# Optimization experiments

Measured on AMD Instinct MI355X. Metric: run time of the kernel, lower is better.

## Reference

```python
import jax, jax.numpy as jnp
import numpy as np

EMBED_DIM = 1024
NUM_HEADS = 16
HEAD_DIM = EMBED_DIM // NUM_HEADS


def setup_inputs() -> dict:
    key = jax.random.key(0)
    ks = jax.random.split(key, 11)
    B, S, E = 4, 2048, EMBED_DIM
    s = 1.0 / np.sqrt(E)
    return {
        "query": jax.random.normal(ks[0], (B, S, E), jnp.float32),
        "key": jax.random.normal(ks[1], (B, S, E), jnp.float32),
        "value": jax.random.normal(ks[2], (B, S, E), jnp.float32),
        "Wq": jax.random.normal(ks[3], (E, E), jnp.float32) * s,
        "bq": jnp.zeros((E,), jnp.float32),
        "Wk": jax.random.normal(ks[4], (E, E), jnp.float32) * s,
        "bk": jnp.zeros((E,), jnp.float32),
        "Wv": jax.random.normal(ks[5], (E, E), jnp.float32) * s,
        "bv": jnp.zeros((E,), jnp.float32),
        "Wo": jax.random.normal(ks[6], (E, E), jnp.float32) * s,
        "bo": jnp.zeros((E,), jnp.float32),
    }


def reference(query, key, value, Wq, bq, Wk, bk, Wv, bv, Wo, bo):
    B, S, E = query.shape
    H, D = NUM_HEADS, HEAD_DIM
    scale = jnp.float32(np.sqrt(D))
    # linear projections (torch Linear: x @ W.T + b)
    Q = (query @ Wq.T + bq).reshape(B, S, H, D).transpose(0, 2, 1, 3)  # [B,H,S,D]
    K = (key @ Wk.T + bk).reshape(B, S, H, D).transpose(0, 2, 1, 3)
    V = (value @ Wv.T + bv).reshape(B, S, H, D).transpose(0, 2, 1, 3)
    # full O(S^2) score materialization, matching the eager torch code
    scores = jnp.einsum("bhqd,bhkd->bhqk", Q, K) / scale  # [B,H,S,S]
    attn = jax.nn.softmax(scores, axis=-1)
    out = jnp.einsum("bhqk,bhkd->bhqd", attn, V)  # [B,H,S,D]
    out = out.transpose(0, 2, 1, 3).reshape(B, S, E)
    out = out @ Wo.T + bo
    return out, attn.mean(axis=1)
```

## Files before the change

### kernel.cpp

```cpp
#include <hip/hip_runtime.h>
#include <hip/hip_bf16.h>

#define DEVI __device__ __forceinline__

typedef __bf16 bf16x8 __attribute__((ext_vector_type(8)));
typedef __bf16 bf16x4 __attribute__((ext_vector_type(4)));
typedef float f32x4 __attribute__((ext_vector_type(4)));

constexpr int B_ = 4, S_ = 2048, E_ = 1024, H_ = 16, D_ = 64;
constexpr int N_ = B_ * S_;
constexpr float SC2_ = 0.18033688011112042f;

constexpr size_t XB_OFF = 0;
constexpr size_t WB_OFF = 50331648;
constexpr size_t QB_OFF = 58720256;
constexpr size_t KB_OFF = 75497472;
constexpr size_t VT_OFF = 92274688;
constexpr size_t CTX_OFF = 109051904;
constexpr size_t LS_OFF = 125829120;
constexpr size_t WS_NEED = 126353408;

typedef const __attribute__((address_space(1))) void* gas_ptr;
typedef __attribute__((address_space(3))) void* las_ptr;

DEVI void load_lds16(const void* g, void* l) {
  __builtin_amdgcn_global_load_lds((gas_ptr)g, (las_ptr)l, 16, 0, 0);
}

DEVI f32x4 mfma16(bf16x8 a, bf16x8 b, f32x4 c) {
  return __builtin_amdgcn_mfma_f32_16x16x32_bf16(a, b, c, 0, 0, 0);
}

DEVI int swz(int row) { return ((row >> 1) ^ (row >> 3)) & 3; }

#if __has_builtin(__builtin_amdgcn_exp2f)
DEVI float ex2(float x) { return __builtin_amdgcn_exp2f(x); }
#else
DEVI float ex2(float x) { return exp2f(x); }
#endif

__global__ __launch_bounds__(256) void conv_x(const float* __restrict__ q,
                                              const float* __restrict__ k,
                                              const float* __restrict__ v,
                                              __bf16* __restrict__ dst) {
  const float* src = (blockIdx.y == 0) ? q : ((blockIdx.y == 1) ? k : v);
  __bf16* d = dst + (size_t)blockIdx.y * N_ * E_;
  size_t i = ((size_t)blockIdx.x * blockDim.x + threadIdx.x) * 4;
  float4 f = *(const float4*)(src + i);
  bf16x4 o;
  o[0] = (__bf16)f.x; o[1] = (__bf16)f.y; o[2] = (__bf16)f.z; o[3] = (__bf16)f.w;
  *(bf16x4*)(d + i) = o;
}

__global__ __launch_bounds__(256) void conv_w(const float* __restrict__ wq,
                                              const float* __restrict__ wk,
                                              const float* __restrict__ wv,
                                              const float* __restrict__ wo,
                                              __bf16* __restrict__ dst) {
  const float* src = (blockIdx.y == 0) ? wq : ((blockIdx.y == 1) ? wk :
                     ((blockIdx.y == 2) ? wv : wo));
  __bf16* d = dst + (size_t)blockIdx.y * E_ * E_;
  size_t i = ((size_t)blockIdx.x * blockDim.x + threadIdx.x) * 4;
  float4 f = *(const float4*)(src + i);
  bf16x4 o;
  o[0] = (__bf16)f.x; o[1] = (__bf16)f.y; o[2] = (__bf16)f.z; o[3] = (__bf16)f.w;
  *(bf16x4*)(d + i) = o;
}

__global__ __launch_bounds__(256) void gemm_qkv(const __bf16* __restrict__ Xb,
                                                const __bf16* __restrict__ Wb,
                                                const float* __restrict__ bq,
                                                const float* __restrict__ bk,
                                                const float* __restrict__ bv,
                                                __bf16* __restrict__ Qb,
                                                __bf16* __restrict__ Kb,
                                                __bf16* __restrict__ Vt) {
  __shared__ __attribute__((aligned(16))) __bf16 As[128 * 32];
  __shared__ __attribute__((aligned(16))) __bf16 Bs[128 * 32];
  const int z = blockIdx.z;
  const __bf16* A = Xb + (size_t)z * N_ * E_;
  const __bf16* W = Wb + (size_t)z * E_ * E_;
  const float* bias = (z == 0) ? bq : ((z == 1) ? bk : bv);
  const int m0 = blockIdx.x * 128, n0 = blockIdx.y * 128;
  const int t = threadIdx.x, lane = t & 63, w = t >> 6;
  const int wm = w >> 1, wn = w & 1;
  const int l15 = lane & 15, g = lane >> 4;

  f32x4 acc[4][4] = {};

  for (int kk = 0; kk < E_; kk += 32) {
#pragma unroll
    for (int i = 0; i < 2; ++i) {
      int c = t + i * 256;
      int row = c >> 2, kc = c & 3;
      int sl = kc ^ swz(row);
      load_lds16(A + (size_t)(m0 + row) * E_ + kk + sl * 8, (void*)(As + c * 8));
      load_lds16(W + (size_t)(n0 + row) * E_ + kk + sl * 8, (void*)(Bs + c * 8));
    }
    __syncthreads();
    bf16x8 a[4], b[4];
#pragma unroll
    for (int i = 0; i < 4; ++i) {
      int row = wm * 64 + i * 16 + l15;
      a[i] = *(const bf16x8*)(As + row * 32 + (g ^ swz(row)) * 8);
    }
#pragma unroll
    for (int j = 0; j < 4; ++j) {
      int row = wn * 64 + j * 16 + l15;
      b[j] = *(const bf16x8*)(Bs + row * 32 + (g ^ swz(row)) * 8);
    }
#pragma unroll
    for (int i = 0; i < 4; ++i)
#pragma unroll
      for (int j = 0; j < 4; ++j)
        acc[i][j] = mfma16(a[i], b[j], acc[i][j]);
    __syncthreads();
  }

#pragma unroll
  for (int i = 0; i < 4; ++i) {
    int mloc = wm * 64 + i * 16 + (g << 2);
#pragma unroll
    for (int j = 0; j < 4; ++j) {
      int nloc = wn * 64 + j * 16 + l15;
      int n = n0 + nloc;
      int h = n >> 6, d = n & 63;
      float bs = bias[n];
      if (z == 2) {
        int m = m0 + mloc;
        int bb = m >> 11, s = m & 2047;
        bf16x4 pk;
#pragma unroll
        for (int r = 0; r < 4; ++r) pk[r] = (__bf16)(acc[i][j][r] + bs);
        *(bf16x4*)(Vt + ((size_t)(bb * H_ + h) * D_ + d) * S_ + s) = pk;
      } else {
        __bf16* dst = (z == 0) ? Qb : Kb;
#pragma unroll
        for (int r = 0; r < 4; ++r) {
          int m = m0 + mloc + r;
          int bb = m >> 11, s = m & 2047;
          dst[((size_t)(bb * H_ + h) * S_ + s) * D_ + d] = (__bf16)(acc[i][j][r] + bs);
        }
      }
    }
  }
}

__global__ __launch_bounds__(256, 4) void attn_pv(const __bf16* __restrict__ Qb,
                                                  const __bf16* __restrict__ Kb,
                                                  const __bf16* __restrict__ Vt,
                                                  float* __restrict__ Lsum,
                                                  __bf16* __restrict__ Ctx) {
  __shared__ __attribute__((aligned(16))) __bf16 Qs[2 * 128 * 32];
  __shared__ __attribute__((aligned(16))) __bf16 Ks[2 * 64 * 32];
  __shared__ __attribute__((aligned(16))) __bf16 Vs[2 * 64 * 32];

  const int q0 = blockIdx.x * 128;
  const int bh = blockIdx.y;
  const __bf16* Qh = Qb + (size_t)bh * S_ * D_;
  const __bf16* Kh = Kb + (size_t)bh * S_ * D_;
  const __bf16* Vh = Vt + (size_t)bh * D_ * S_;
  const int t = threadIdx.x, lane = t & 63, w = t >> 6;
  const int l15 = lane & 15, g = lane >> 4;
  const int ksel = 8 * (l15 >> 2) + (l15 & 3);

#pragma unroll
  for (int i = 0; i < 4; ++i) {
    int c = t + i * 256;
    int sub = c >> 9, rem = c & 511, row = rem >> 2, kc = rem & 3;
    int sl = kc ^ swz(row);
    load_lds16(Qh + (size_t)(q0 + row) * D_ + sub * 32 + sl * 8, (void*)(Qs + c * 8));
  }
  __syncthreads();
  bf16x8 qf[2][2];
#pragma unroll
  for (int jb = 0; jb < 2; ++jb) {
    int row = w * 32 + jb * 16 + l15;
#pragma unroll
    for (int ks = 0; ks < 2; ++ks)
      qf[jb][ks] = *(const bf16x8*)(Qs + ks * 4096 + row * 32 + (g ^ swz(row)) * 8);
  }

  bf16x8 ones;
#pragma unroll
  for (int i = 0; i < 8; ++i) ones[i] = (__bf16)1.0f;

  f32x4 acc[4][2] = {};
  f32x4 lacc[2] = {};

  for (int k0 = 0; k0 < S_; k0 += 64) {
#pragma unroll
    for (int i = 0; i < 2; ++i) {
      int c = t + i * 256;
      int sub = c >> 8, rem = c & 255, row = rem >> 2, kc = rem & 3;
      int sl = kc ^ swz(row);
      load_lds16(Kh + (size_t)(k0 + row) * D_ + sub * 32 + sl * 8, (void*)(Ks + c * 8));
      load_lds16(Vh + (size_t)row * S_ + k0 + sub * 32 + sl * 8, (void*)(Vs + c * 8));
    }
    __syncthreads();

#pragma unroll
    for (int chunk = 0; chunk < 2; ++chunk) {
      f32x4 sc[2][2];
#pragma unroll
      for (int blk = 0; blk < 2; ++blk) {
        int krow = chunk * 32 + 4 * blk + ksel;
        int so = (g ^ swz(krow)) * 8;
        bf16x8 kf0 = *(const bf16x8*)(Ks + krow * 32 + so);
        bf16x8 kf1 = *(const bf16x8*)(Ks + 2048 + krow * 32 + so);
#pragma unroll
        for (int jb = 0; jb < 2; ++jb) {
          f32x4 s = {};
          s = mfma16(kf0, qf[jb][0], s);
          s = mfma16(kf1, qf[jb][1], s);
          sc[blk][jb] = s;
        }
      }
      bf16x8 pf[2];
#pragma unroll
      for (int jb = 0; jb < 2; ++jb) {
#pragma unroll
        for (int r = 0; r < 4; ++r) {
          pf[jb][r]     = (__bf16)ex2(sc[0][jb][r] * SC2_);
          pf[jb][4 + r] = (__bf16)ex2(sc[1][jb][r] * SC2_);
        }
        lacc[jb] = mfma16(ones, pf[jb], lacc[jb]);
      }
#pragma unroll
      for (int mb = 0; mb < 4; ++mb) {
        int row = mb * 16 + l15;
        bf16x8 vf = *(const bf16x8*)(Vs + chunk * 2048 + row * 32 + (g ^ swz(row)) * 8);
#pragma unroll
        for (int jb = 0; jb < 2; ++jb)
          acc[mb][jb] = mfma16(vf, pf[jb], acc[mb][jb]);
      }
    }
    __syncthreads();
  }

  if (lane < 16) {
#pragma unroll
    for (int jb = 0; jb < 2; ++jb)
      Lsum[(size_t)bh * S_ + q0 + w * 32 + jb * 16 + lane] = lacc[jb][0];
  }

  const int bb = bh >> 4, h = bh & 15;
#pragma unroll
  for (int jb = 0; jb < 2; ++jb) {
    float invl = 1.0f / lacc[jb][0];
    int q = q0 + w * 32 + jb * 16 + l15;
#pragma unroll
    for (int mb = 0; mb < 4; ++mb) {
      int d = mb * 16 + (g << 2);
      bf16x4 pk;
#pragma unroll
      for (int r = 0; r < 4; ++r) pk[r] = (__bf16)(acc[mb][jb][r] * invl);
      *(bf16x4*)(Ctx + ((size_t)bb * S_ + q) * E_ + h * 64 + d) = pk;
    }
  }
}

__global__ __launch_bounds__(256, 4) void attn_mean(const __bf16* __restrict__ Qb,
                                                    const __bf16* __restrict__ Kb,
                                                    const float* __restrict__ Lsum,
                                                    float* __restrict__ meanout) {
  __shared__ __attribute__((aligned(16))) __bf16 Qs[2 * 128 * 32];
  __shared__ __attribute__((aligned(16))) __bf16 Ks2[2 * 128 * 32];
  const int k0 = blockIdx.x * 128, q0 = blockIdx.y * 128, bI = blockIdx.z;
  const int t = threadIdx.x, lane = t & 63, w = t >> 6;
  const int l15 = lane & 15, g = lane >> 4;
  const int ksel = 8 * (l15 >> 2) + (l15 & 3);

  f32x4 macc[4][2][2] = {};

  for (int h = 0; h < H_; ++h) {
    const size_t bh = (size_t)bI * H_ + h;
    const __bf16* Qh = Qb + bh * S_ * D_;
    const __bf16* Kh = Kb + bh * S_ * D_;
#pragma unroll
    for (int i = 0; i < 4; ++i) {
      int c = t + i * 256;
      int sub = c >> 9, rem = c & 511, row = rem >> 2, kc = rem & 3;
      int sl = kc ^ swz(row);
      load_lds16(Qh + (size_t)(q0 + row) * D_ + sub * 32 + sl * 8, (void*)(Qs + c * 8));
      load_lds16(Kh + (size_t)(k0 + row) * D_ + sub * 32 + sl * 8, (void*)(Ks2 + c * 8));
    }
    float invl[2];
#pragma unroll
    for (int jb = 0; jb < 2; ++jb)
      invl[jb] = 1.0f / Lsum[bh * S_ + q0 + w * 32 + jb * 16 + l15];
    __syncthreads();

    bf16x8 qf[2][2];
#pragma unroll
    for (int jb = 0; jb < 2; ++jb) {
      int row = w * 32 + jb * 16 + l15;
#pragma unroll
      for (int ks = 0; ks < 2; ++ks)
        qf[jb][ks] = *(const bf16x8*)(Qs + ks * 4096 + row * 32 + (g ^ swz(row)) * 8);
    }

#pragma unroll
    for (int chunk = 0; chunk < 4; ++chunk) {
#pragma unroll
      for (int blk = 0; blk < 2; ++blk) {
        int krow = chunk * 32 + 4 * blk + ksel;
        int so = (g ^ swz(krow)) * 8;
        bf16x8 kf0 = *(const bf16x8*)(Ks2 + krow * 32 + so);
        bf16x8 kf1 = *(const bf16x8*)(Ks2 + 4096 + krow * 32 + so);
#pragma unroll
        for (int jb = 0; jb < 2; ++jb) {
          f32x4 s = {};
          s = mfma16(kf0, qf[jb][0], s);
          s = mfma16(kf1, qf[jb][1], s);
#pragma unroll
          for (int r = 0; r < 4; ++r)
            macc[chunk][blk][jb][r] += ex2(s[r] * SC2_) * invl[jb];
        }
      }
    }
    __syncthreads();
  }

#pragma unroll
  for (int chunk = 0; chunk < 4; ++chunk)
#pragma unroll
    for (int blk = 0; blk < 2; ++blk)
#pragma unroll
      for (int jb = 0; jb < 2; ++jb) {
        int q = q0 + w * 32 + jb * 16 + l15;
        int kb = k0 + chunk * 32 + 8 * g + 4 * blk;
        f32x4 o;
#pragma unroll
        for (int r = 0; r < 4; ++r) o[r] = macc[chunk][blk][jb][r] * 0.0625f;
        *(f32x4*)(meanout + ((size_t)bI * S_ + q) * S_ + kb) = o;
      }
}

__global__ __launch_bounds__(256) void gemm_out(const __bf16* __restrict__ Ctx,
                                                const __bf16* __restrict__ Wo,
                                                const float* __restrict__ bo,
                                                float* __restrict__ out) {
  __shared__ __attribute__((aligned(16))) __bf16 As[128 * 32];
  __shared__ __attribute__((aligned(16))) __bf16 Bs[128 * 32];
  const int m0 = blockIdx.x * 128, n0 = blockIdx.y * 128;
  const int t = threadIdx.x, lane = t & 63, w = t >> 6;
  const int wm = w >> 1, wn = w & 1;
  const int l15 = lane & 15, g = lane >> 4;

  f32x4 acc[4][4] = {};

  for (int kk = 0; kk < E_; kk += 32) {
#pragma unroll
    for (int i = 0; i < 2; ++i) {
      int c = t + i * 256;
      int row = c >> 2, kc = c & 3;
      int sl = kc ^ swz(row);
      load_lds16(Ctx + (size_t)(m0 + row) * E_ + kk + sl * 8, (void*)(As + c * 8));
      load_lds16(Wo + (size_t)(n0 + row) * E_ + kk + sl * 8, (void*)(Bs + c * 8));
    }
    __syncthreads();
    bf16x8 a[4], b[4];
#pragma unroll
    for (int i = 0; i < 4; ++i) {
      int row = wm * 64 + i * 16 + l15;
      a[i] = *(const bf16x8*)(As + row * 32 + (g ^ swz(row)) * 8);
    }
#pragma unroll
    for (int j = 0; j < 4; ++j) {
      int row = wn * 64 + j * 16 + l15;
      b[j] = *(const bf16x8*)(Bs + row * 32 + (g ^ swz(row)) * 8);
    }
#pragma unroll
    for (int i = 0; i < 4; ++i)
#pragma unroll
      for (int j = 0; j < 4; ++j)
        acc[i][j] = mfma16(a[i], b[j], acc[i][j]);
    __syncthreads();
  }

#pragma unroll
  for (int i = 0; i < 4; ++i) {
    int mloc = wm * 64 + i * 16 + (g << 2);
#pragma unroll
    for (int j = 0; j < 4; ++j) {
      int n = n0 + wn * 64 + j * 16 + l15;
      float bs = bo[n];
#pragma unroll
      for (int r = 0; r < 4; ++r)
        out[(size_t)(m0 + mloc + r) * E_ + n] = acc[i][j][r] + bs;
    }
  }
}

extern "C" void kernel_launch(void* const* d_in, const int* in_sizes, int n_in,
                              void* d_out, int out_size, void* d_ws, size_t ws_size,
                              hipStream_t stream) {
  if (ws_size < WS_NEED) {
    hipMemsetAsync(d_out, 0, (size_t)out_size * sizeof(float), stream);
    return;
  }

  const float* q  = (const float*)d_in[0];
  const float* k  = (const float*)d_in[1];
  const float* v  = (const float*)d_in[2];
  const float* Wq = (const float*)d_in[3];
  const float* bq = (const float*)d_in[4];
  const float* Wk = (const float*)d_in[5];
  const float* bk = (const float*)d_in[6];
  const float* Wv = (const float*)d_in[7];
  const float* bv = (const float*)d_in[8];
  const float* Wo = (const float*)d_in[9];
  const float* bo = (const float*)d_in[10];

  char* ws = (char*)d_ws;
  __bf16* Xb  = (__bf16*)(ws + XB_OFF);
  __bf16* Wb  = (__bf16*)(ws + WB_OFF);
  __bf16* Qb  = (__bf16*)(ws + QB_OFF);
  __bf16* Kb  = (__bf16*)(ws + KB_OFF);
  __bf16* Vt  = (__bf16*)(ws + VT_OFF);
  __bf16* Ctx = (__bf16*)(ws + CTX_OFF);
  float*  Ls  = (float*)(ws + LS_OFF);

  float* out0 = (float*)d_out;
  float* out1 = (float*)d_out + (size_t)N_ * E_;

  conv_x<<<dim3(N_ * E_ / 4 / 256, 3), 256, 0, stream>>>(q, k, v, Xb);
  conv_w<<<dim3(E_ * E_ / 4 / 256, 4), 256, 0, stream>>>(Wq, Wk, Wv, Wo, Wb);
  gemm_qkv<<<dim3(N_ / 128, E_ / 128, 3), 256, 0, stream>>>(Xb, Wb, bq, bk, bv, Qb, Kb, Vt);
  attn_pv<<<dim3(S_ / 128, B_ * H_), 256, 0, stream>>>(Qb, Kb, Vt, Ls, Ctx);
  attn_mean<<<dim3(S_ / 128, S_ / 128, B_), 256, 0, stream>>>(Qb, Kb, Ls, out1);
  gemm_out<<<dim3(N_ / 128, E_ / 128), 256, 0, stream>>>(Ctx, Wb + 3 * (size_t)E_ * E_, bo, out0);
}
```

Baseline: 432.0 us.

## Double-buffer K/V in attention and fuse attn_mean with output GEMM

```diff
diff --git a/kernel.cpp b/kernel.cpp
--- a/kernel.cpp
+++ b/kernel.cpp
@@ -151,9 +151,7 @@
                                                   const __bf16* __restrict__ Vt,
                                                   float* __restrict__ Lsum,
                                                   __bf16* __restrict__ Ctx) {
-  __shared__ __attribute__((aligned(16))) __bf16 Qs[2 * 128 * 32];
-  __shared__ __attribute__((aligned(16))) __bf16 Ks[2 * 64 * 32];
-  __shared__ __attribute__((aligned(16))) __bf16 Vs[2 * 64 * 32];
+  __shared__ __attribute__((aligned(16))) __bf16 smem[2][8192];
 
   const int q0 = blockIdx.x * 128;
   const int bh = blockIdx.y;
@@ -164,21 +162,13 @@
   const int l15 = lane & 15, g = lane >> 4;
   const int ksel = 8 * (l15 >> 2) + (l15 & 3);
 
-#pragma unroll
-  for (int i = 0; i < 4; ++i) {
-    int c = t + i * 256;
-    int sub = c >> 9, rem = c & 511, row = rem >> 2, kc = rem & 3;
-    int sl = kc ^ swz(row);
-    load_lds16(Qh + (size_t)(q0 + row) * D_ + sub * 32 + sl * 8, (void*)(Qs + c * 8));
-  }
-  __syncthreads();
   bf16x8 qf[2][2];
 #pragma unroll
   for (int jb = 0; jb < 2; ++jb) {
     int row = w * 32 + jb * 16 + l15;
 #pragma unroll
     for (int ks = 0; ks < 2; ++ks)
-      qf[jb][ks] = *(const bf16x8*)(Qs + ks * 4096 + row * 32 + (g ^ swz(row)) * 8);
+      qf[jb][ks] = *(const bf16x8*)(Qh + (size_t)(q0 + row) * D_ + ks * 32 + g * 8);
   }
 
   bf16x8 ones;
@@ -188,17 +178,19 @@
   f32x4 acc[4][2] = {};
   f32x4 lacc[2] = {};
 
-  for (int k0 = 0; k0 < S_; k0 += 64) {
+  auto stage_kv = [&](int kk0, __bf16* buf) {
 #pragma unroll
     for (int i = 0; i < 2; ++i) {
       int c = t + i * 256;
       int sub = c >> 8, rem = c & 255, row = rem >> 2, kc = rem & 3;
       int sl = kc ^ swz(row);
-      load_lds16(Kh + (size_t)(k0 + row) * D_ + sub * 32 + sl * 8, (void*)(Ks + c * 8));
-      load_lds16(Vh + (size_t)row * S_ + k0 + sub * 32 + sl * 8, (void*)(Vs + c * 8));
-    }
-    __syncthreads();
-
+      load_lds16(Kh + (size_t)(kk0 + row) * D_ + sub * 32 + sl * 8, (void*)(buf + c * 8));
+      load_lds16(Vh + (size_t)row * S_ + kk0 + sub * 32 + sl * 8, (void*)(buf + 4096 + c * 8));
+    }
+  };
+
+  auto compute = [&](const __bf16* Ksb) {
+    const __bf16* Vsb = Ksb + 4096;
 #pragma unroll
     for (int chunk = 0; chunk < 2; ++chunk) {
       f32x4 sc[2][2];
@@ -206,8 +198,8 @@
       for (int blk = 0; blk < 2; ++blk) {
         int krow = chunk * 32 + 4 * blk + ksel;
         int so = (g ^ swz(krow)) * 8;
-        bf16x8 kf0 = *(const bf16x8*)(Ks + krow * 32 + so);
-        bf16x8 kf1 = *(const bf16x8*)(Ks + 2048 + krow * 32 + so);
+        bf16x8 kf0 = *(const bf16x8*)(Ksb + krow * 32 + so);
+        bf16x8 kf1 = *(const bf16x8*)(Ksb + 2048 + krow * 32 + so);
 #pragma unroll
         for (int jb = 0; jb < 2; ++jb) {
           f32x4 s = {};
@@ -226,17 +218,35 @@
         }
         lacc[jb] = mfma16(ones, pf[jb], lacc[jb]);
       }
+      __builtin_amdgcn_s_setprio(1);
 #pragma unroll
       for (int mb = 0; mb < 4; ++mb) {
         int row = mb * 16 + l15;
-        bf16x8 vf = *(const bf16x8*)(Vs + chunk * 2048 + row * 32 + (g ^ swz(row)) * 8);
+        bf16x8 vf = *(const bf16x8*)(Vsb + chunk * 2048 + row * 32 + (g ^ swz(row)) * 8);
 #pragma unroll
         for (int jb = 0; jb < 2; ++jb)
           acc[mb][jb] = mfma16(vf, pf[jb], acc[mb][jb]);
       }
-    }
-    __syncthreads();
-  }
+      __builtin_amdgcn_s_setprio(0);
+    }
+  };
+
+  stage_kv(0, smem[0]);
+  stage_kv(64, smem[1]);
+
+  for (int tt = 0; tt < 30; ++tt) {
+    asm volatile("s_waitcnt vmcnt(4)" ::: "memory");
+    __builtin_amdgcn_s_barrier();
+    compute(smem[tt & 1]);
+    __builtin_amdgcn_s_barrier();
+    stage_kv((tt + 2) * 64, smem[tt & 1]);
+  }
+  asm volatile("s_waitcnt vmcnt(4)" ::: "memory");
+  __builtin_amdgcn_s_barrier();
+  compute(smem[0]);
+  asm volatile("s_waitcnt vmcnt(0)" ::: "memory");
+  __builtin_amdgcn_s_barrier();
+  compute(smem[1]);
 
   if (lane < 16) {
 #pragma unroll
@@ -260,13 +270,17 @@
   }
 }
 
-__global__ __launch_bounds__(256, 4) void attn_mean(const __bf16* __restrict__ Qb,
-                                                    const __bf16* __restrict__ Kb,
-                                                    const float* __restrict__ Lsum,
-                                                    float* __restrict__ meanout) {
-  __shared__ __attribute__((aligned(16))) __bf16 Qs[2 * 128 * 32];
-  __shared__ __attribute__((aligned(16))) __bf16 Ks2[2 * 128 * 32];
-  const int k0 = blockIdx.x * 128, q0 = blockIdx.y * 128, bI = blockIdx.z;
+
+DEVI void attn_mean_body(int id, __bf16* smem,
+                         const __bf16* __restrict__ Qb,
+                         const __bf16* __restrict__ Kb,
+                         const float* __restrict__ Lsum,
+                         float* __restrict__ meanout) {
+  __bf16* Qs  = smem;
+  __bf16* Ks2 = smem + 8192;
+  const int k0 = (id & 15) * 128;
+  const int q0 = ((id >> 4) & 15) * 128;
+  const int bI = id >> 8;
   const int t = threadIdx.x, lane = t & 63, w = t >> 6;
   const int l15 = lane & 15, g = lane >> 4;
   const int ksel = 8 * (l15 >> 2) + (l15 & 3);
@@ -337,13 +351,14 @@
       }
 }
 
-__global__ __launch_bounds__(256) void gemm_out(const __bf16* __restrict__ Ctx,
-                                                const __bf16* __restrict__ Wo,
-                                                const float* __restrict__ bo,
-                                                float* __restrict__ out) {
-  __shared__ __attribute__((aligned(16))) __bf16 As[128 * 32];
-  __shared__ __attribute__((aligned(16))) __bf16 Bs[128 * 32];
-  const int m0 = blockIdx.x * 128, n0 = blockIdx.y * 128;
+DEVI void gemm_out_body(int id, __bf16* smem,
+                        const __bf16* __restrict__ Ctx,
+                        const __bf16* __restrict__ Wo,
+                        const float* __restrict__ bo,
+                        float* __restrict__ out) {
+  __bf16* As = smem;
+  __bf16* Bs = smem + 4096;
+  const int m0 = (id & 63) * 128, n0 = (id >> 6) * 128;
   const int t = threadIdx.x, lane = t & 63, w = t >> 6;
   const int wm = w >> 1, wn = w & 1;
   const int l15 = lane & 15, g = lane >> 4;
@@ -391,6 +406,23 @@
         out[(size_t)(m0 + mloc + r) * E_ + n] = acc[i][j][r] + bs;
     }
   }
+}
+
+__global__ __launch_bounds__(256, 3) void tail_fused(const __bf16* __restrict__ Qb,
+                                                     const __bf16* __restrict__ Kb,
+                                                     const float* __restrict__ Lsum,
+                                                     float* __restrict__ meanout,
+                                                     const __bf16* __restrict__ Ctx,
+                                                     const __bf16* __restrict__ Wo,
+                                                     const float* __restrict__ bo,
+                                                     float* __restrict__ out) {
+  __shared__ __attribute__((aligned(16))) __bf16 smem[16384];
+  const int bid = blockIdx.x;
+  const int g3 = bid / 3, r3 = bid - g3 * 3;
+  if (r3 == 2)
+    gemm_out_body(g3, smem, Ctx, Wo, bo, out);
+  else
+    attn_mean_body(2 * g3 + r3, smem, Qb, Kb, Lsum, meanout);
 }
 
 extern "C" void kernel_launch(void* const* d_in, const int* in_sizes, int n_in,
@@ -429,6 +461,6 @@
   conv_w<<<dim3(E_ * E_ / 4 / 256, 4), 256, 0, stream>>>(Wq, Wk, Wv, Wo, Wb);
   gemm_qkv<<<dim3(N_ / 128, E_ / 128, 3), 256, 0, stream>>>(Xb, Wb, bq, bk, bv, Qb, Kb, Vt);
   attn_pv<<<dim3(S_ / 128, B_ * H_), 256, 0, stream>>>(Qb, Kb, Vt, Ls, Ctx);
-  attn_mean<<<dim3(S_ / 128, S_ / 128, B_), 256, 0, stream>>>(Qb, Kb, Ls, out1);
-  gemm_out<<<dim3(N_ / 128, E_ / 128), 256, 0, stream>>>(Ctx, Wb + 3 * (size_t)E_ * E_, bo, out0);
-}
+  tail_fused<<<dim3(1536), 256, 0, stream>>>(Qb, Kb, Ls, out1, Ctx,
+                                             Wb + 3 * (size_t)E_ * E_, bo, out0);
+}
```

Result: no change. 430.0 us (-0.5%).
